# Kernel tuning notes

Measured on AMD Instinct MI355X. Metric: run time of the kernel, lower is better.

## Reference

```python
import jax, jax.numpy as jnp
import numpy as np

N_NODES = 100000
N_EDGES = 1600000
IN_DIM, HID_DIM, OUT_DIM = 128, 64, 64
NEG_SLOPE = 0.2


def _gat_layer(h_in, src, dst, W, a_src, a_dst, b, n_nodes):
    # h: [N, F_out]
    h = h_in @ W.T
    alpha_src = h @ a_src  # [N]
    alpha_dst = h @ a_dst  # [N]
    # per-edge raw attention logits (edge j->i: src=j, dst=i)
    e = jax.nn.leaky_relu(alpha_src[src] + alpha_dst[dst], NEG_SLOPE)  # [E]
    # segment softmax over incoming edges of each dst node
    m = jax.ops.segment_max(e, dst, num_segments=n_nodes)
    ex = jnp.exp(e - m[dst])
    denom = jax.ops.segment_sum(ex, dst, num_segments=n_nodes)
    alpha = ex / denom[dst]  # [E], denom > 0 thanks to self-loops
    out = jax.ops.segment_sum(h[src] * alpha[:, None], dst, num_segments=n_nodes)
    return out + b


def setup_inputs() -> dict:
    key = jax.random.key(0)
    ks = jax.random.split(key, 12)
    x = jax.random.normal(ks[0], (N_NODES, IN_DIM), dtype=jnp.float32)
    edge_index = jax.random.randint(ks[1], (2, N_EDGES), 0, N_NODES)
    edge_attr = jax.random.normal(ks[2], (N_EDGES, 1), dtype=jnp.float32)
    s1 = 1.0 / np.sqrt(IN_DIM)
    s2 = 1.0 / np.sqrt(HID_DIM)
    W1 = jax.random.normal(ks[3], (HID_DIM, IN_DIM), dtype=jnp.float32) * s1
    att_src1 = jax.random.normal(ks[4], (HID_DIM,), dtype=jnp.float32) * s2
    att_dst1 = jax.random.normal(ks[5], (HID_DIM,), dtype=jnp.float32) * s2
    b1 = jnp.zeros((HID_DIM,), dtype=jnp.float32)
    W2 = jax.random.normal(ks[6], (OUT_DIM, HID_DIM), dtype=jnp.float32) * s2
    att_src2 = jax.random.normal(ks[7], (OUT_DIM,), dtype=jnp.float32) * s2
    att_dst2 = jax.random.normal(ks[8], (OUT_DIM,), dtype=jnp.float32) * s2
    b2 = jnp.zeros((OUT_DIM,), dtype=jnp.float32)
    return {"x": x, "edge_index": edge_index, "edge_attr": edge_attr,
            "W1": W1, "att_src1": att_src1, "att_dst1": att_dst1, "b1": b1,
            "W2": W2, "att_src2": att_src2, "att_dst2": att_dst2, "b2": b2}


def reference(x, edge_index, edge_attr, W1, att_src1, att_dst1, b1,
              W2, att_src2, att_dst2, b2):
    n = x.shape[0]
    # add self-loops (PyG GATConv default); edge_attr unused (edge_dim=None)
    loop = jnp.arange(n, dtype=edge_index.dtype)
    src = jnp.concatenate([edge_index[0], loop])
    dst = jnp.concatenate([edge_index[1], loop])
    h = _gat_layer(x, src, dst, W1, att_src1, att_dst1, b1, n)
    h = jax.nn.relu(h)
    h = _gat_layer(h, src, dst, W2, att_src2, att_dst2, b2, n)
    # global_mean_pool with batch=None -> mean over all nodes, shape [1, F]
    return jnp.mean(h, axis=0, keepdims=True)
```

## Files before the change

kernel.cpp:

```cpp
#include <hip/hip_runtime.h>

#define NEG_SLOPE 0.2f
#define BSHIFT 6
#define NBMAX 2048
#define BCAP 1408
#define ESTRIDE (BCAP + 64)
#define CHUNK 4096

typedef __attribute__((ext_vector_type(8))) short short8;
typedef __attribute__((ext_vector_type(4))) float f32x4;

__device__ __forceinline__ unsigned short f2b(float x) {
    unsigned u = __float_as_uint(x);
    u += 0x7fff + ((u >> 16) & 1);
    return (unsigned short)(u >> 16);
}
__device__ __forceinline__ float b2f(unsigned short u) {
    return __uint_as_float((unsigned)u << 16);
}

__global__ __launch_bounds__(256) void hist_kernel(
    const int* __restrict__ ei, int* __restrict__ hist, int E, int NB)
{
    __shared__ int cnt[NBMAX];
    const int tid = threadIdx.x;
    for (int i = tid; i < NB; i += 256) cnt[i] = 0;
    __syncthreads();
    const int start = blockIdx.x * CHUNK;
    const int end = min(start + CHUNK, E);
    int i = start + tid;
    for (; i + 7 * 256 < end; i += 8 * 256) {
        int dv[8];
        #pragma unroll
        for (int j = 0; j < 8; ++j) dv[j] = ei[E + i + j * 256];
        #pragma unroll
        for (int j = 0; j < 8; ++j) atomicAdd(&cnt[dv[j] >> BSHIFT], 1);
    }
    for (; i < end; i += 256)
        atomicAdd(&cnt[ei[E + i] >> BSHIFT], 1);
    __syncthreads();
    for (int k = tid; k < NB; k += 256)
        hist[(size_t)blockIdx.x * NB + k] = cnt[k];
}

__global__ __launch_bounds__(256) void colscan_kernel(
    int* __restrict__ hist, int* __restrict__ btotal, int NB, int NBLK)
{
    const int col = (int)((blockIdx.x * 256 + threadIdx.x) >> 6);
    const int ln  = threadIdx.x & 63;
    if (col >= NB) return;
    int run = 0;
    for (int r0 = 0; r0 < NBLK; r0 += 64) {
        const int r = r0 + ln;
        const bool ok = (r < NBLK);
        int v = ok ? hist[(size_t)r * NB + col] : 0;
        int inc = v;
        #pragma unroll
        for (int off = 1; off < 64; off <<= 1) {
            int x = __shfl_up(inc, off, 64);
            if (ln >= off) inc += x;
        }
        if (ok) hist[(size_t)r * NB + col] = run + inc - v;
        run += __shfl(inc, 63, 64);
    }
    if (ln == 0) btotal[col] = run;
}

template<int K, bool BF16IN>
__device__ __forceinline__ void gemm_attn_core(
    unsigned short* __restrict__ xb, unsigned short* __restrict__ wb,
    float* __restrict__ avs, float* __restrict__ avd, int bid,
    const void* __restrict__ in_v, const float* __restrict__ W,
    const float* __restrict__ a_src, const float* __restrict__ a_dst,
    unsigned short* __restrict__ hb, float* __restrict__ asrc,
    float* __restrict__ adst, int N)
{
    constexpr int LDK = K + 8;
    const int tid = threadIdx.x;
    const int node0 = bid * 64;
    const int w = tid >> 6;
    const int lane = tid & 63;
    const int col = lane & 15;
    const int quad = lane >> 4;

    if (tid < 64) { avs[tid] = a_src[tid]; avd[tid] = a_dst[tid]; }

    for (int i = tid; i < 64 * (K / 4); i += 256) {
        int r = i / (K / 4), c = i % (K / 4);
        float4 v = *(const float4*)&W[(size_t)r * K + 4 * c];
        *(ushort4*)&wb[r * LDK + 4 * c] =
            make_ushort4(f2b(v.x), f2b(v.y), f2b(v.z), f2b(v.w));
    }
    if (BF16IN) {
        const unsigned short* in = (const unsigned short*)in_v;
        for (int i = tid; i < 64 * (K / 8); i += 256) {
            int r = i / (K / 8), c = i % (K / 8);
            int node = node0 + r;
            ulonglong2 v = (node < N)
                ? *(const ulonglong2*)&in[(size_t)node * K + 8 * c]
                : make_ulonglong2(0ull, 0ull);
            *(ulonglong2*)&xb[r * LDK + 8 * c] = v;
        }
    } else {
        const float* in = (const float*)in_v;
        for (int i = tid; i < 64 * (K / 4); i += 256) {
            int r = i / (K / 4), c = i % (K / 4);
            int node = node0 + r;
            float4 v = (node < N) ? *(const float4*)&in[(size_t)node * K + 4 * c]
                                  : make_float4(0.f, 0.f, 0.f, 0.f);
            *(ushort4*)&xb[r * LDK + 4 * c] =
                make_ushort4(f2b(v.x), f2b(v.y), f2b(v.z), f2b(v.w));
        }
    }
    __syncthreads();

    f32x4 acc[4] = {f32x4{0,0,0,0}, f32x4{0,0,0,0}, f32x4{0,0,0,0}, f32x4{0,0,0,0}};
    #pragma unroll
    for (int kc = 0; kc < K / 32; ++kc) {
        short8 a = *(const short8*)&xb[(16 * w + col) * LDK + kc * 32 + quad * 8];
        #pragma unroll
        for (int j = 0; j < 4; ++j) {
            short8 b = *(const short8*)&wb[(16 * j + col) * LDK + kc * 32 + quad * 8];
            acc[j] = __builtin_amdgcn_mfma_f32_16x16x32_bf16(a, b, acc[j], 0, 0, 0);
        }
    }

    #pragma unroll
    for (int r = 0; r < 4; ++r) {
        const int node = node0 + 16 * w + quad * 4 + r;
        const bool valid = node < N;
        float vs = 0.f, vd = 0.f;
        #pragma unroll
        for (int j = 0; j < 4; ++j) {
            float hv = acc[j][r];
            int f = 16 * j + col;
            if (valid) hb[(size_t)node * 64 + f] = f2b(hv);
            vs = fmaf(hv, avs[f], vs);
            vd = fmaf(hv, avd[f], vd);
        }
        #pragma unroll
        for (int off = 8; off >= 1; off >>= 1) {
            vs += __shfl_down(vs, off, 16);
            vd += __shfl_down(vd, off, 16);
        }
        if (col == 0 && valid) { asrc[node] = vs; adst[node] = vd; }
    }
}

__global__ __launch_bounds__(256) void scatter_gemm_kernel(
    const int* __restrict__ ei, const int* __restrict__ hist,
    int* __restrict__ binned, int E, int NB, int nblk,
    const float* __restrict__ x, const float* __restrict__ W1,
    const float* __restrict__ as1, const float* __restrict__ ad1,
    unsigned short* __restrict__ hb, float* __restrict__ asrc,
    float* __restrict__ adst, int N)
{
    extern __shared__ char smem[];
    if ((int)blockIdx.x < nblk) {
        int* base = (int*)smem;
        int* cnt2 = base + NBMAX;
        const int q = nblk >> 3, rr = nblk & 7;
        const int xs = blockIdx.x & 7, k = blockIdx.x >> 3;
        const int chunk = ((xs < rr) ? xs * (q + 1) : rr * (q + 1) + (xs - rr) * q) + k;
        const int tid = threadIdx.x;
        for (int i = tid; i < NB; i += 256) {
            base[i] = hist[(size_t)chunk * NB + i];
            cnt2[i] = 0;
        }
        __syncthreads();
        const int start = chunk * CHUNK;
        const int end = min(start + CHUNK, E);
        int i = start + tid;
        for (; i + 7 * 256 < end; i += 8 * 256) {
            int sv[8], dv[8];
            #pragma unroll
            for (int j = 0; j < 8; ++j) {
                sv[j] = ei[i + j * 256];
                dv[j] = ei[E + i + j * 256];
            }
            #pragma unroll
            for (int j = 0; j < 8; ++j) {
                int b = dv[j] >> BSHIFT;
                int r = base[b] + atomicAdd(&cnt2[b], 1);
                if (r < BCAP)
                    binned[(size_t)b * BCAP + r] = (sv[j] << BSHIFT) | (dv[j] & 63);
            }
        }
        for (; i < end; i += 256) {
            int s = ei[i], d = ei[E + i];
            int b = d >> BSHIFT;
            int r = base[b] + atomicAdd(&cnt2[b], 1);
            if (r < BCAP) binned[(size_t)b * BCAP + r] = (s << BSHIFT) | (d & 63);
        }
    } else {
        constexpr int LDK = 128 + 8;
        unsigned short* xb = (unsigned short*)smem;
        unsigned short* wb = xb + 64 * LDK;
        float* avs = (float*)(wb + 64 * LDK);
        float* avd = avs + 64;
        gemm_attn_core<128, false>(xb, wb, avs, avd, (int)blockIdx.x - nblk,
                                   x, W1, as1, ad1, hb, asrc, adst, N);
    }
}

__global__ __launch_bounds__(256) void bucket_csr_kernel(
    const int* __restrict__ binned, const int* __restrict__ btotal,
    int* __restrict__ row_ptr, int* __restrict__ rend,
    int* __restrict__ esrc, int N)
{
    __shared__ int ldeg[64];
    __shared__ int lcur[64];
    const int b = blockIdx.x;
    const int tid = threadIdx.x;
    const int node0 = b << BSHIFT;
    const int cnt = min(btotal[b], BCAP);
    const int base_e = b * ESTRIDE;
    const int* bp = binned + (size_t)b * BCAP;

    if (tid < 64) ldeg[tid] = (node0 + tid < N) ? 1 : 0;
    __syncthreads();
    for (int i = tid; i < cnt; i += 256)
        atomicAdd(&ldeg[bp[i] & 63], 1);
    __syncthreads();
    if (tid < 64) {
        int v = ldeg[tid];
        int inc = v;
        #pragma unroll
        for (int off = 1; off < 64; off <<= 1) {
            int t2 = __shfl_up(inc, off, 64);
            if (tid >= off) inc += t2;
        }
        int excl = inc - v;
        int node = node0 + tid;
        if (node < N) {
            row_ptr[node] = base_e + excl;
            rend[node] = base_e + excl + v;
            esrc[base_e + excl] = node;
            lcur[tid] = base_e + excl + 1;
        }
    }
    __syncthreads();
    for (int i = tid; i < cnt; i += 256) {
        int v = bp[i];
        int pos = atomicAdd(&lcur[v & 63], 1);
        esrc[pos] = v >> BSHIFT;
    }
}

template<int K, bool BF16IN>
__global__ __launch_bounds__(256) void gemm_attn_kernel(
    const void* __restrict__ in_v, const float* __restrict__ W,
    const float* __restrict__ a_src, const float* __restrict__ a_dst,
    unsigned short* __restrict__ hb, float* __restrict__ asrc,
    float* __restrict__ adst, int N)
{
    constexpr int LDK = K + 8;
    __shared__ unsigned short xb[64 * LDK];
    __shared__ unsigned short wb[64 * LDK];
    __shared__ float avs[64], avd[64];
    gemm_attn_core<K, BF16IN>(xb, wb, avs, avd, (int)blockIdx.x,
                              in_v, W, a_src, a_dst, hb, asrc, adst, N);
}

__global__ __launch_bounds__(256) void aggregate_csr_kernel(
    const int* __restrict__ row_ptr, const int* __restrict__ rend,
    const int* __restrict__ esrc,
    const float* __restrict__ asrc, const float* __restrict__ adst,
    const unsigned short* __restrict__ hb, const float* __restrict__ bias,
    unsigned short* __restrict__ gb, int N, int do_relu)
{
    const int node = (int)((blockIdx.x * 256 + threadIdx.x) >> 4);
    const int lane = threadIdx.x & 15;
    if (node >= N) return;
    const int beg = row_ptr[node];
    const int end = rend[node];
    const float ad = adst[node];
    float a0 = 0.f, a1 = 0.f, a2 = 0.f, a3 = 0.f, wsum = 0.f;
    int p = beg;
    for (; p + 4 <= end; p += 4) {
        int s[4]; ushort4 r[4]; float l[4];
        #pragma unroll
        for (int j = 0; j < 4; ++j) s[j] = esrc[p + j];
        #pragma unroll
        for (int j = 0; j < 4; ++j)
            r[j] = *(const ushort4*)(hb + (size_t)s[j] * 64 + lane * 4);
        #pragma unroll
        for (int j = 0; j < 4; ++j) l[j] = asrc[s[j]] + ad;
        #pragma unroll
        for (int j = 0; j < 4; ++j) {
            float ll = (l[j] > 0.f) ? l[j] : NEG_SLOPE * l[j];
            float w = __expf(ll);
            wsum += w;
            a0 = fmaf(w, b2f(r[j].x), a0);
            a1 = fmaf(w, b2f(r[j].y), a1);
            a2 = fmaf(w, b2f(r[j].z), a2);
            a3 = fmaf(w, b2f(r[j].w), a3);
        }
    }
    for (; p < end; ++p) {
        int s = esrc[p];
        ushort4 r = *(const ushort4*)(hb + (size_t)s * 64 + lane * 4);
        float l = asrc[s] + ad;
        l = (l > 0.f) ? l : NEG_SLOPE * l;
        float w = __expf(l);
        wsum += w;
        a0 = fmaf(w, b2f(r.x), a0);
        a1 = fmaf(w, b2f(r.y), a1);
        a2 = fmaf(w, b2f(r.z), a2);
        a3 = fmaf(w, b2f(r.w), a3);
    }
    const float inv = 1.0f / wsum;
    float4 v = make_float4(a0 * inv, a1 * inv, a2 * inv, a3 * inv);
    if (bias) {
        v.x += bias[lane * 4 + 0]; v.y += bias[lane * 4 + 1];
        v.z += bias[lane * 4 + 2]; v.w += bias[lane * 4 + 3];
    }
    if (do_relu) {
        v.x = fmaxf(v.x, 0.f); v.y = fmaxf(v.y, 0.f);
        v.z = fmaxf(v.z, 0.f); v.w = fmaxf(v.w, 0.f);
    }
    *(ushort4*)&gb[(size_t)node * 64 + lane * 4] =
        make_ushort4(f2b(v.x), f2b(v.y), f2b(v.z), f2b(v.w));
}

__global__ __launch_bounds__(256) void pool_kernel(
    const unsigned short* __restrict__ gb, const float* __restrict__ b2,
    float* __restrict__ out, int N)
{
    __shared__ float red[256];
    const int f = threadIdx.x & 63;
    const int sub = threadIdx.x >> 6;
    float acc = 0.f;
    for (int n = blockIdx.x * 4 + sub; n < N; n += gridDim.x * 4)
        acc += b2f(gb[(size_t)n * 64 + f]);
    red[threadIdx.x] = acc;
    __syncthreads();
    if (threadIdx.x < 64) {
        float s = red[f] + red[64 + f] + red[128 + f] + red[192 + f];
        atomicAdd(out + f, s * (1.0f / (float)N));
        if (blockIdx.x == 0) atomicAdd(out + f, b2[f]);
    }
}

extern "C" void kernel_launch(void* const* d_in, const int* in_sizes, int n_in,
                              void* d_out, int out_size, void* d_ws, size_t ws_size,
                              hipStream_t stream) {
    const float* x   = (const float*)d_in[0];
    const int*   ei  = (const int*)d_in[1];
    const float* W1  = (const float*)d_in[3];
    const float* as1 = (const float*)d_in[4];
    const float* ad1 = (const float*)d_in[5];
    const float* b1  = (const float*)d_in[6];
    const float* W2  = (const float*)d_in[7];
    const float* as2 = (const float*)d_in[8];
    const float* ad2 = (const float*)d_in[9];
    const float* b2  = (const float*)d_in[10];
    float* out = (float*)d_out;

    const int N = in_sizes[0] / 128;
    const int E = in_sizes[1] / 2;
    const int NB = (N + 63) >> BSHIFT;
    const int NBLK = (E + CHUNK - 1) / CHUNK;

    auto align4 = [](size_t v) { return (v + 3) & ~(size_t)3; };
    float* ws    = (float*)d_ws;
    size_t off = 0;
    unsigned short* hb = (unsigned short*)(ws + off); off += align4((size_t)N * 32);
    unsigned short* gb = (unsigned short*)(ws + off); off += align4((size_t)N * 32);
    float* asrc  = ws + off; off += align4(N);
    float* adst  = ws + off; off += align4(N);
    int* row_ptr = (int*)(ws + off); off += align4(N);
    int* rend    = (int*)(ws + off); off += align4(N);
    int* btotal  = (int*)(ws + off); off += NBMAX;
    int* hist    = (int*)(ws + off); off += align4((size_t)NBLK * NB);
    int* esrc    = (int*)(ws + off); off += align4((size_t)NB * ESTRIDE);
    int* binned  = (int*)gb;

    const int gemm_blocks = (N + 63) / 64;
    const int agg_blocks  = (int)(((size_t)N * 16 + 255) / 256);
    const int packed_lds  = 64 * (128 + 8) * 2 * 2 + 2 * 64 * 4;

    hipMemsetAsync(out, 0, 64 * sizeof(float), stream);

    hist_kernel<<<NBLK, 256, 0, stream>>>(ei, hist, E, NB);
    colscan_kernel<<<(NB * 64 + 255) / 256, 256, 0, stream>>>(hist, btotal, NB, NBLK);
    scatter_gemm_kernel<<<NBLK + gemm_blocks, 256, packed_lds, stream>>>(
        ei, hist, binned, E, NB, NBLK, x, W1, as1, ad1, hb, asrc, adst, N);
    bucket_csr_kernel<<<NB, 256, 0, stream>>>(binned, btotal, row_ptr, rend, esrc, N);

    aggregate_csr_kernel<<<agg_blocks, 256, 0, stream>>>(
        row_ptr, rend, esrc, asrc, adst, hb, b1, gb, N, 1);

    gemm_attn_kernel<64, true><<<gemm_blocks, 256, 0, stream>>>(
        gb, W2, as2, ad2, hb, asrc, adst, N);
    aggregate_csr_kernel<<<agg_blocks, 256, 0, stream>>>(
        row_ptr, rend, esrc, asrc, adst, hb, nullptr, gb, N, 0);

    pool_kernel<<<512, 256, 0, stream>>>(gb, b2, out, N);
}
```

Measured before the change: 270.0 us.

## Phase-sort CSR edges by source range and use persistent grid for aggregation

The CSR build now groups each destination's incoming edges by source-node phase (src>>13, 16 phases), so edges are ordered by source range within every row. Aggregation switches to a grid-stride persistent loop over 2048 blocks. Together the aim is for concurrently running blocks to gather from nearby regions of hb and asrc, improving L2 locality of the random gathers. The cost is a larger shared-memory counter array and more atomics in bucket_csr, and locality only helps if blocks stay roughly in step.

```diff
diff --git a/kernel.cpp b/kernel.cpp
--- a/kernel.cpp
+++ b/kernel.cpp
@@ -6,6 +6,9 @@
 #define BCAP 1408
 #define ESTRIDE (BCAP + 64)
 #define CHUNK 4096
+#define PSHIFT 13
+#define NPHASE 16
+#define AGG_GRID 2048
 
 typedef __attribute__((ext_vector_type(8))) short short8;
 typedef __attribute__((ext_vector_type(4))) float f32x4;
@@ -208,42 +211,56 @@
     int* __restrict__ row_ptr, int* __restrict__ rend,
     int* __restrict__ esrc, int N)
 {
-    __shared__ int ldeg[64];
-    __shared__ int lcur[64];
+    __shared__ int cnt[64][NPHASE];
+    __shared__ int lcur[64][NPHASE];
     const int b = blockIdx.x;
     const int tid = threadIdx.x;
     const int node0 = b << BSHIFT;
-    const int cnt = min(btotal[b], BCAP);
+    const int cntE = min(btotal[b], BCAP);
     const int base_e = b * ESTRIDE;
     const int* bp = binned + (size_t)b * BCAP;
 
-    if (tid < 64) ldeg[tid] = (node0 + tid < N) ? 1 : 0;
-    __syncthreads();
-    for (int i = tid; i < cnt; i += 256)
-        atomicAdd(&ldeg[bp[i] & 63], 1);
+    for (int i = tid; i < 64 * NPHASE; i += 256) ((int*)cnt)[i] = 0;
+    __syncthreads();
+    if (tid < 64 && node0 + tid < N)
+        cnt[tid][(node0 + tid) >> PSHIFT] = 1;
+    __syncthreads();
+    for (int i = tid; i < cntE; i += 256) {
+        int v = bp[i];
+        atomicAdd(&cnt[v & 63][(v >> BSHIFT) >> PSHIFT], 1);
+    }
     __syncthreads();
     if (tid < 64) {
-        int v = ldeg[tid];
-        int inc = v;
+        int tot = 0;
+        #pragma unroll
+        for (int ph = 0; ph < NPHASE; ++ph) tot += cnt[tid][ph];
+        int inc = tot;
         #pragma unroll
         for (int off = 1; off < 64; off <<= 1) {
             int t2 = __shfl_up(inc, off, 64);
             if (tid >= off) inc += t2;
         }
-        int excl = inc - v;
-        int node = node0 + tid;
+        int base = base_e + inc - tot;
+        const int node = node0 + tid;
         if (node < N) {
-            row_ptr[node] = base_e + excl;
-            rend[node] = base_e + excl + v;
-            esrc[base_e + excl] = node;
-            lcur[tid] = base_e + excl + 1;
-        }
-    }
-    __syncthreads();
-    for (int i = tid; i < cnt; i += 256) {
+            row_ptr[node] = base;
+            rend[node] = base + tot;
+            int off2 = base;
+            #pragma unroll
+            for (int ph = 0; ph < NPHASE; ++ph) {
+                lcur[tid][ph] = off2;
+                off2 += cnt[tid][ph];
+            }
+            int sph = node >> PSHIFT;
+            esrc[lcur[tid][sph]++] = node;
+        }
+    }
+    __syncthreads();
+    for (int i = tid; i < cntE; i += 256) {
         int v = bp[i];
-        int pos = atomicAdd(&lcur[v & 63], 1);
-        esrc[pos] = v >> BSHIFT;
+        int src = v >> BSHIFT;
+        int pos = atomicAdd(&lcur[v & 63][src >> PSHIFT], 1);
+        esrc[pos] = src;
     }
 }
 
@@ -269,58 +286,63 @@
     const unsigned short* __restrict__ hb, const float* __restrict__ bias,
     unsigned short* __restrict__ gb, int N, int do_relu)
 {
-    const int node = (int)((blockIdx.x * 256 + threadIdx.x) >> 4);
+    const int slot = threadIdx.x >> 4;
     const int lane = threadIdx.x & 15;
-    if (node >= N) return;
-    const int beg = row_ptr[node];
-    const int end = rend[node];
-    const float ad = adst[node];
-    float a0 = 0.f, a1 = 0.f, a2 = 0.f, a3 = 0.f, wsum = 0.f;
-    int p = beg;
-    for (; p + 4 <= end; p += 4) {
-        int s[4]; ushort4 r[4]; float l[4];
-        #pragma unroll
-        for (int j = 0; j < 4; ++j) s[j] = esrc[p + j];
-        #pragma unroll
-        for (int j = 0; j < 4; ++j)
-            r[j] = *(const ushort4*)(hb + (size_t)s[j] * 64 + lane * 4);
-        #pragma unroll
-        for (int j = 0; j < 4; ++j) l[j] = asrc[s[j]] + ad;
-        #pragma unroll
-        for (int j = 0; j < 4; ++j) {
-            float ll = (l[j] > 0.f) ? l[j] : NEG_SLOPE * l[j];
-            float w = __expf(ll);
+    const int ngroups = (N + 15) >> 4;
+
+    for (int g = blockIdx.x; g < ngroups; g += gridDim.x) {
+        const int node = g * 16 + slot;
+        if (node >= N) continue;
+        const int beg = row_ptr[node];
+        const int end = rend[node];
+        const float ad = adst[node];
+        float a0 = 0.f, a1 = 0.f, a2 = 0.f, a3 = 0.f, wsum = 0.f;
+        int p = beg;
+        for (; p + 4 <= end; p += 4) {
+            int s[4]; ushort4 r[4]; float l[4];
+            #pragma unroll
+            for (int j = 0; j < 4; ++j) s[j] = esrc[p + j];
+            #pragma unroll
+            for (int j = 0; j < 4; ++j)
+                r[j] = *(const ushort4*)(hb + (size_t)s[j] * 64 + lane * 4);
+            #pragma unroll
+            for (int j = 0; j < 4; ++j) l[j] = asrc[s[j]] + ad;
+            #pragma unroll
+            for (int j = 0; j < 4; ++j) {
+                float ll = (l[j] > 0.f) ? l[j] : NEG_SLOPE * l[j];
+                float w = __expf(ll);
+                wsum += w;
+                a0 = fmaf(w, b2f(r[j].x), a0);
+                a1 = fmaf(w, b2f(r[j].y), a1);
+                a2 = fmaf(w, b2f(r[j].z), a2);
+                a3 = fmaf(w, b2f(r[j].w), a3);
+            }
+        }
+        for (; p < end; ++p) {
+            int s = esrc[p];
+            ushort4 r = *(const ushort4*)(hb + (size_t)s * 64 + lane * 4);
+            float l = asrc[s] + ad;
+            l = (l > 0.f) ? l : NEG_SLOPE * l;
+            float w = __expf(l);
             wsum += w;
-            a0 = fmaf(w, b2f(r[j].x), a0);
-            a1 = fmaf(w, b2f(r[j].y), a1);
-            a2 = fmaf(w, b2f(r[j].z), a2);
-            a3 = fmaf(w, b2f(r[j].w), a3);
-        }
-    }
-    for (; p < end; ++p) {
-        int s = esrc[p];
-        ushort4 r = *(const ushort4*)(hb + (size_t)s * 64 + lane * 4);
-        float l = asrc[s] + ad;
-        l = (l > 0.f) ? l : NEG_SLOPE * l;
-        float w = __expf(l);
-        wsum += w;
-        a0 = fmaf(w, b2f(r.x), a0);
-        a1 = fmaf(w, b2f(r.y), a1);
-        a2 = fmaf(w, b2f(r.z), a2);
-        a3 = fmaf(w, b2f(r.w), a3);
-    }
-    const float inv = 1.0f / wsum;
-    float4 v = make_float4(a0 * inv, a1 * inv, a2 * inv, a3 * inv);
-    if (bias) {
-        v.x += bias[lane * 4 + 0]; v.y += bias[lane * 4 + 1];
-        v.z += bias[lane * 4 + 2]; v.w += bias[lane * 4 + 3];
-    }
-    if (do_relu) {
-        v.x = fmaxf(v.x, 0.f); v.y = fmaxf(v.y, 0.f);
-        v.z = fmaxf(v.z, 0.f); v.w = fmaxf(v.w, 0.f);
-    }
-    *(ushort4*)&gb[(size_t)node * 64 + lane * 4] =
-        make_ushort4(f2b(v.x), f2b(v.y), f2b(v.z), f2b(v.w));
+            a0 = fmaf(w, b2f(r.x), a0);
+            a1 = fmaf(w, b2f(r.y), a1);
+            a2 = fmaf(w, b2f(r.z), a2);
+            a3 = fmaf(w, b2f(r.w), a3);
+        }
+        const float inv = 1.0f / wsum;
+        float4 v = make_float4(a0 * inv, a1 * inv, a2 * inv, a3 * inv);
+        if (bias) {
+            v.x += bias[lane * 4 + 0]; v.y += bias[lane * 4 + 1];
+            v.z += bias[lane * 4 + 2]; v.w += bias[lane * 4 + 3];
+        }
+        if (do_relu) {
+            v.x = fmaxf(v.x, 0.f); v.y = fmaxf(v.y, 0.f);
+            v.z = fmaxf(v.z, 0.f); v.w = fmaxf(v.w, 0.f);
+        }
+        *(ushort4*)&gb[(size_t)node * 64 + lane * 4] =
+            make_ushort4(f2b(v.x), f2b(v.y), f2b(v.z), f2b(v.w));
+    }
 }
 
 __global__ __launch_bounds__(256) void pool_kernel(
@@ -377,7 +399,6 @@
     int* binned  = (int*)gb;
 
     const int gemm_blocks = (N + 63) / 64;
-    const int agg_blocks  = (int)(((size_t)N * 16 + 255) / 256);
     const int packed_lds  = 64 * (128 + 8) * 2 * 2 + 2 * 64 * 4;
 
     hipMemsetAsync(out, 0, 64 * sizeof(float), stream);
@@ -388,12 +409,12 @@
         ei, hist, binned, E, NB, NBLK, x, W1, as1, ad1, hb, asrc, adst, N);
     bucket_csr_kernel<<<NB, 256, 0, stream>>>(binned, btotal, row_ptr, rend, esrc, N);
 
-    aggregate_csr_kernel<<<agg_blocks, 256, 0, stream>>>(
+    aggregate_csr_kernel<<<AGG_GRID, 256, 0, stream>>>(
         row_ptr, rend, esrc, asrc, adst, hb, b1, gb, N, 1);
 
     gemm_attn_kernel<64, true><<<gemm_blocks, 256, 0, stream>>>(
         gb, W2, as2, ad2, hb, asrc, adst, N);
-    aggregate_csr_kernel<<<agg_blocks, 256, 0, stream>>>(
+    aggregate_csr_kernel<<<AGG_GRID, 256, 0, stream>>>(
         row_ptr, rend, esrc, asrc, adst, hb, nullptr, gb, N, 0);
 
     pool_kernel<<<512, 256, 0, stream>>>(gb, b2, out, N);
```

Measured after the change: 271.8 us. Within noise of the previous version (+0.7%).
